# Kernel optimization log

Measured on AMD Instinct MI355X. Metric: run time of the kernel, lower is better.

The kernel has to match this reference:

```python
import jax, jax.numpy as jnp
import numpy as np

T, B, E = 2048, 2, 1024
H = 16
D = E // H


def setup_inputs() -> dict:
    key = jax.random.key(0)
    ks = jax.random.split(key, 7)
    s = 1.0 / np.sqrt(E)
    return {
        "query": jax.random.normal(ks[0], (T, B, E), jnp.float32),
        "key": jax.random.normal(ks[1], (T, B, E), jnp.float32),
        "value": jax.random.normal(ks[2], (T, B, E), jnp.float32),
        "in_proj_weight": jax.random.normal(ks[3], (3 * E, E), jnp.float32) * s,
        "in_proj_bias": jax.random.normal(ks[4], (3 * E,), jnp.float32) * 0.02,
        "out_proj_weight": jax.random.normal(ks[5], (E, E), jnp.float32) * s,
        "out_proj_bias": jax.random.normal(ks[6], (E,), jnp.float32) * 0.02,
    }


def reference(query, key, value, in_proj_weight, in_proj_bias, out_proj_weight, out_proj_bias):
    tgt_len, bsz, embed_dim = query.shape
    src_len = key.shape[0]
    head_dim = embed_dim // H
    # packed in-projection (F.linear: x @ W.T + b)
    w_q, w_k, w_v = jnp.split(in_proj_weight, 3, axis=0)
    b_q, b_k, b_v = jnp.split(in_proj_bias, 3, axis=0)
    q = query @ w_q.T + b_q   # [T, B, E]
    k = key @ w_k.T + b_k     # [S, B, E]
    v = value @ w_v.T + b_v   # [S, B, E]
    # [T,B,E] -> [B,H,T,D]
    q = q.reshape(tgt_len, bsz, H, head_dim).transpose(1, 2, 0, 3)
    k = k.reshape(src_len, bsz, H, head_dim).transpose(1, 2, 0, 3)
    v = v.reshape(src_len, bsz, H, head_dim).transpose(1, 2, 0, 3)
    scale = 1.0 / jnp.sqrt(jnp.asarray(head_dim, q.dtype))
    scores = jnp.einsum("bhtd,bhsd->bhts", q, k) * scale  # [B,H,T,S]
    attn_weights = jax.nn.softmax(scores, axis=-1)
    attn = jnp.einsum("bhts,bhsd->bhtd", attn_weights, v)  # [B,H,T,D]
    # [B,H,T,D] -> [T,B,E]
    attn = attn.transpose(2, 0, 1, 3).reshape(tgt_len, bsz, embed_dim)
    attn_output = attn @ out_proj_weight.T + out_proj_bias  # [T,B,E]
    # averaged attention weights over heads (average_attn_weights=True)
    avg_weights = jnp.sum(attn_weights, axis=1) / H  # [B,T,S]
    return attn_output, avg_weights
```

## Files before the change

kernel.cpp:

```cpp
#include <hip/hip_runtime.h>
#include <hip/hip_bf16.h>

typedef float  f32x2  __attribute__((ext_vector_type(2)));
typedef float  f32x4  __attribute__((ext_vector_type(4)));
typedef float  f32x16 __attribute__((ext_vector_type(16)));
typedef __bf16 bf16x8 __attribute__((ext_vector_type(8)));

#define MFMA16(A,B,C) __builtin_amdgcn_mfma_f32_16x16x32_bf16((A),(B),(C),0,0,0)
#define MFMA32(A,B,C) __builtin_amdgcn_mfma_f32_32x32x16_bf16((A),(B),(C),0,0,0)
#define EXP2(x) __builtin_amdgcn_exp2f(x)
#define LOG2(x) __builtin_amdgcn_logf(x)

static constexpr int Tn = 2048, Bn = 2, En = 1024, Hn = 16, Dn = 64;
static constexpr float kQScale = 0.125f * 1.4426950408889634f;

static __device__ __forceinline__ unsigned pack2(float a, float b) {
  union { __bf16 h[2]; unsigned u; } un;
  un.h[0] = (__bf16)a; un.h[1] = (__bf16)b;
  return un.u;
}

static __device__ __forceinline__ void gload_lds16(const void* g, void* l) {
  __builtin_amdgcn_global_load_lds(
      (const __attribute__((address_space(1))) void*)g,
      (__attribute__((address_space(3))) void*)l, 16, 0, 0);
}

__global__ __launch_bounds__(256)
void k_cvt(const float* __restrict__ q, const float* __restrict__ k,
           const float* __restrict__ v, const float* __restrict__ w3,
           const float* __restrict__ wo,
           __bf16* __restrict__ qb, __bf16* __restrict__ kb,
           __bf16* __restrict__ vb, __bf16* __restrict__ w3b,
           __bf16* __restrict__ wob)
{
  const size_t g = (size_t)blockIdx.x * 256 + threadIdx.x;
  const float* src;
  __bf16* dst;
  size_t off;
  if (g < 524288)        { src = q;  dst = qb;  off = g; }
  else if (g < 1048576)  { src = k;  dst = kb;  off = g - 524288; }
  else if (g < 1572864)  { src = v;  dst = vb;  off = g - 1048576; }
  else if (g < 1966080)  { src = w3; dst = w3b; off = g - 1572864; }
  else                   { src = wo; dst = wob; off = g - 1966080; }
  const float* p = src + off * 8;
  f32x4 a = *reinterpret_cast<const f32x4*>(p);
  f32x4 b = *reinterpret_cast<const f32x4*>(p + 4);
  bf16x8 o;
  #pragma unroll
  for (int e = 0; e < 4; ++e) { o[e] = (__bf16)a[e]; o[e + 4] = (__bf16)b[e]; }
  *reinterpret_cast<bf16x8*>(dst + off * 8) = o;
}

__global__ __launch_bounds__(256)
void k_qkv(const __bf16* __restrict__ Xq, const __bf16* __restrict__ Xk,
           const __bf16* __restrict__ Xv, const __bf16* __restrict__ W,
           const float* __restrict__ bias,
           __bf16* __restrict__ q_ws, __bf16* __restrict__ k_ws,
           __bf16* __restrict__ v_ws)
{
  __shared__ __align__(16) char a_lds[8192];
  __shared__ __align__(16) char b_lds[8192];
  const int tid = threadIdx.x;
  const int lane = tid & 63, w = tid >> 6;
  const int wr = w >> 1, wc = w & 1;
  const int ag = lane >> 4, lr = lane & 15;
  const int mBase = blockIdx.x * 128;
  const int oBase = blockIdx.y * 128;
  const int which = blockIdx.y >> 3;
  const __bf16* X  = (which == 0) ? Xq : ((which == 1) ? Xk : Xv);
  const __bf16* Wt = W + (size_t)oBase * En;
  __bf16* dst = (which == 0) ? q_ws : ((which == 1) ? k_ws : v_ws);
  const float oscale = (which == 0) ? kQScale : 1.0f;

  const int g0 = w >> 1, h0 = w & 1;
  const int gA = w;
  char* laA0 = a_lds + gA * 2048;
  char* laA1 = a_lds + gA * 2048 + 1024;
  char* lbA0 = b_lds + gA * 2048;
  char* lbA1 = b_lds + gA * 2048 + 1024;
  const __bf16* pa0 = X  + (size_t)(mBase + lane) * En + gA * 8;
  const __bf16* pa1 = X  + (size_t)(mBase + 64 + lane) * En + gA * 8;
  const __bf16* pb0 = Wt + (size_t)(lane) * En + gA * 8;
  const __bf16* pb1 = Wt + (size_t)(64 + lane) * En + gA * 8;
  (void)g0; (void)h0;

  f32x4 acc[4][4];
  #pragma unroll
  for (int i = 0; i < 4; ++i)
    #pragma unroll
    for (int j = 0; j < 4; ++j) { f32x4 z = {0.f, 0.f, 0.f, 0.f}; acc[i][j] = z; }

  for (int kk = 0; kk < En; kk += 32) {
    __syncthreads();
    gload_lds16(pa0 + kk, laA0);
    gload_lds16(pa1 + kk, laA1);
    gload_lds16(pb0 + kk, lbA0);
    gload_lds16(pb1 + kk, lbA1);
    __syncthreads();
    bf16x8 af[4], bfr[4];
    #pragma unroll
    for (int mb = 0; mb < 4; ++mb)
      af[mb] = *(const bf16x8*)(a_lds + ag * 2048 + (wr * 64 + mb * 16 + lr) * 16);
    #pragma unroll
    for (int nb = 0; nb < 4; ++nb)
      bfr[nb] = *(const bf16x8*)(b_lds + ag * 2048 + (wc * 64 + nb * 16 + lr) * 16);
    #pragma unroll
    for (int mb = 0; mb < 4; ++mb)
      #pragma unroll
      for (int nb = 0; nb < 4; ++nb)
        acc[mb][nb] = MFMA16(af[mb], bfr[nb], acc[mb][nb]);
  }

  #pragma unroll
  for (int nb = 0; nb < 4; ++nb) {
    int oG = oBase + wc * 64 + nb * 16 + lr;
    float bv = bias[oG];
    int oS = oG & (En - 1);
    int h = oS >> 6, d = oS & 63;
    #pragma unroll
    for (int mb = 0; mb < 4; ++mb)
      #pragma unroll
      for (int r = 0; r < 4; ++r) {
        int i = mBase + wr * 64 + mb * 16 + ag * 4 + r;
        int t = i >> 1, b2 = i & 1;
        dst[(((size_t)(b2 * Hn + h)) * Tn + t) * Dn + d] =
            (__bf16)((acc[mb][nb][r] + bv) * oscale);
      }
  }
}

__global__ __launch_bounds__(256)
void k_transpose_v(const __bf16* __restrict__ v_ws, __bf16* __restrict__ vt_ws)
{
  __shared__ __bf16 tile[64][72];
  const int bh = blockIdx.x >> 5;
  const int tt = blockIdx.x & 31;
  const int tid = threadIdx.x;
  const __bf16* src = v_ws + ((size_t)bh * Tn + tt * 64) * Dn;
  #pragma unroll
  for (int it = 0; it < 2; ++it) {
    int gi = tid + it * 256;
    int row = gi >> 3, gg = gi & 7;
    *reinterpret_cast<bf16x8*>(&tile[row][gg * 8]) =
        *reinterpret_cast<const bf16x8*>(src + row * Dn + gg * 8);
  }
  __syncthreads();
  __bf16* dst = vt_ws + (size_t)bh * Dn * Tn + tt * 64;
  #pragma unroll
  for (int it = 0; it < 2; ++it) {
    int gi = tid + it * 256;
    int drow = gi >> 3, tg = gi & 7;
    bf16x8 vv;
    #pragma unroll
    for (int e = 0; e < 8; ++e) vv[e] = tile[tg * 8 + e][drow];
    *reinterpret_cast<bf16x8*>(dst + (size_t)drow * Tn + tg * 8) = vv;
  }
}

__global__ __launch_bounds__(256, 2)
void k_flash(const __bf16* __restrict__ q_ws, const __bf16* __restrict__ k_ws,
             const __bf16* __restrict__ vt_ws, __bf16* __restrict__ ctx,
             float* __restrict__ stats)
{
  __shared__ __align__(16) char k_sm[8192];
  __shared__ __align__(16) char v_sm[8192];
  __shared__ __align__(16) float es_sm[4][32];

  const int tid = threadIdx.x;
  const int lane = tid & 63, w = tid >> 6;
  const int tl = lane & 31, hi = lane >> 5;
  const int bh = blockIdx.x >> 4;
  const int qt = blockIdx.x & 15;
  const int t0w = qt * 128 + w * 32;

  const __bf16* kbase  = k_ws + (size_t)bh * Tn * Dn;
  const __bf16* vtbase = vt_ws + (size_t)bh * Dn * Tn;

  bf16x8 qf[4];
  {
    const __bf16* qrow = q_ws + ((size_t)bh * Tn + t0w + tl) * Dn + hi * 8;
    #pragma unroll
    for (int c = 0; c < 4; ++c)
      qf[c] = *reinterpret_cast<const bf16x8*>(qrow + c * 16);
  }

  f32x16 accO0, accO1;
  #pragma unroll
  for (int i = 0; i < 16; ++i) { accO0[i] = 0.f; accO1[i] = 0.f; }
  float m_run = -INFINITY, l_run = 0.f;

  const int r0 = tid >> 3, s0 = tid & 7;
  const int ldso = ((s0 ^ (r0 & 7)) << 4);
  const int ko0 = r0 * 128 + ldso, ko1 = ko0 + 32 * 128;

  bf16x8 rk0 = *(const bf16x8*)(kbase + r0 * 64 + s0 * 8);
  bf16x8 rk1 = *(const bf16x8*)(kbase + (r0 + 32) * 64 + s0 * 8);
  bf16x8 rv0 = *(const bf16x8*)(vtbase + (size_t)r0 * Tn + s0 * 8);
  bf16x8 rv1 = *(const bf16x8*)(vtbase + (size_t)(r0 + 32) * Tn + s0 * 8);

  for (int st = 0; st < 32; ++st) {
    __syncthreads();
    *(bf16x8*)(k_sm + ko0) = rk0;
    *(bf16x8*)(k_sm + ko1) = rk1;
    *(bf16x8*)(v_sm + ko0) = rv0;
    *(bf16x8*)(v_sm + ko1) = rv1;
    __syncthreads();
    if (st + 1 < 32) {
      const __bf16* kn = kbase + (size_t)(st + 1) * 64 * Dn;
      const __bf16* vn = vtbase + (st + 1) * 64;
      rk0 = *(const bf16x8*)(kn + r0 * 64 + s0 * 8);
      rk1 = *(const bf16x8*)(kn + (r0 + 32) * 64 + s0 * 8);
      rv0 = *(const bf16x8*)(vn + (size_t)r0 * Tn + s0 * 8);
      rv1 = *(const bf16x8*)(vn + (size_t)(r0 + 32) * Tn + s0 * 8);
    }

    f32x16 sc0, sc1;
    #pragma unroll
    for (int i = 0; i < 16; ++i) { sc0[i] = 0.f; sc1[i] = 0.f; }
    const char* kr0 = k_sm + tl * 128;
    const char* kr1 = k_sm + (32 + tl) * 128;
    #pragma unroll
    for (int c = 0; c < 4; ++c) {
      const int off = (((2 * c + hi) ^ (tl & 7)) << 4);
      sc0 = MFMA32(*(const bf16x8*)(kr0 + off), qf[c], sc0);
      sc1 = MFMA32(*(const bf16x8*)(kr1 + off), qf[c], sc1);
    }

    float mx[8];
    #pragma unroll
    for (int i = 0; i < 8; ++i)
      mx[i] = fmaxf(fmaxf(sc0[i], sc0[i + 8]), fmaxf(sc1[i], sc1[i + 8]));
    float tm = fmaxf(fmaxf(fmaxf(mx[0], mx[1]), fmaxf(mx[2], mx[3])),
                     fmaxf(fmaxf(mx[4], mx[5]), fmaxf(mx[6], mx[7])));
    tm = fmaxf(tm, __shfl_xor(tm, 32, 64));
    const float mn = fmaxf(m_run, tm);
    const float es = EXP2(m_run - mn);
    m_run = mn;
    #pragma unroll
    for (int i = 0; i < 16; ++i) {
      sc0[i] = EXP2(sc0[i] - mn);
      sc1[i] = EXP2(sc1[i] - mn);
    }
    float p0s = 0.f, p1s = 0.f, p2s = 0.f, p3s = 0.f;
    #pragma unroll
    for (int i = 0; i < 16; i += 4) {
      p0s += sc0[i]     + sc1[i];
      p1s += sc0[i + 1] + sc1[i + 1];
      p2s += sc0[i + 2] + sc1[i + 2];
      p3s += sc0[i + 3] + sc1[i + 3];
    }
    float rs = (p0s + p1s) + (p2s + p3s);
    rs += __shfl_xor(rs, 32, 64);
    l_run = l_run * es + rs;

    es_sm[w][tl] = es;
    f32x4 esr[4];
    #pragma unroll
    for (int q = 0; q < 4; ++q)
      esr[q] = *(const f32x4*)&es_sm[w][8 * q + 4 * hi];
    #pragma unroll
    for (int q = 0; q < 4; ++q)
      #pragma unroll
      for (int rr = 0; rr < 4; ++rr) {
        accO0[q * 4 + rr] *= esr[q][rr];
        accO1[q * 4 + rr] *= esr[q][rr];
      }

    unsigned wA0[4], wB0[4], wA1[4], wB1[4];
    #pragma unroll
    for (int g = 0; g < 4; ++g) {
      wA0[g] = pack2(sc0[4 * g],     sc0[4 * g + 1]);
      wB0[g] = pack2(sc0[4 * g + 2], sc0[4 * g + 3]);
      wA1[g] = pack2(sc1[4 * g],     sc1[4 * g + 1]);
      wB1[g] = pack2(sc1[4 * g + 2], sc1[4 * g + 3]);
    }
    bf16x8 pa[2][2];
    #pragma unroll
    for (int sb = 0; sb < 2; ++sb) {
      const unsigned* WA = sb ? wA1 : wA0;
      const unsigned* WB = sb ? wB1 : wB0;
      #pragma unroll
      for (int c = 0; c < 2; ++c) {
        unsigned a0 = WA[2 * c], a1 = WA[2 * c + 1];
        unsigned b0 = WB[2 * c], b1 = WB[2 * c + 1];
        unsigned xa0 = __shfl_xor(a0, 32, 64);
        unsigned xa1 = __shfl_xor(a1, 32, 64);
        unsigned xb0 = __shfl_xor(b0, 32, 64);
        unsigned xb1 = __shfl_xor(b1, 32, 64);
        union { unsigned u[4]; bf16x8 v; } uu;
        uu.u[0] = hi ? xa1 : a0;
        uu.u[1] = hi ? xb1 : b0;
        uu.u[2] = hi ? a1 : xa0;
        uu.u[3] = hi ? b1 : xb0;
        pa[sb][c] = uu.v;
      }
    }

    const char* vr0 = v_sm + tl * 128;
    const char* vr1 = v_sm + (32 + tl) * 128;
    #pragma unroll
    for (int sb = 0; sb < 2; ++sb)
      #pragma unroll
      for (int c = 0; c < 2; ++c) {
        const int off = (((sb * 4 + c * 2 + hi) ^ (tl & 7)) << 4);
        accO0 = MFMA32(pa[sb][c], *(const bf16x8*)(vr0 + off), accO0);
        accO1 = MFMA32(pa[sb][c], *(const bf16x8*)(vr1 + off), accO1);
      }
  }

  const float linv = 1.0f / l_run;
  es_sm[w][tl] = linv;
  f32x4 lr[4];
  #pragma unroll
  for (int q = 0; q < 4; ++q)
    lr[q] = *(const f32x4*)&es_sm[w][8 * q + 4 * hi];
  const int b2 = bh >> 4, h = bh & 15;
  #pragma unroll
  for (int q = 0; q < 4; ++q)
    #pragma unroll
    for (int rr = 0; rr < 4; ++rr) {
      const int t = t0w + 8 * q + 4 * hi + rr;
      __bf16* cp = ctx + ((size_t)t * Bn + b2) * En + h * 64 + tl;
      cp[0]  = (__bf16)(accO0[q * 4 + rr] * lr[q][rr]);
      cp[32] = (__bf16)(accO1[q * 4 + rr] * lr[q][rr]);
    }
  if (hi == 0) {
    const int t = t0w + tl;
    f32x2 stv; stv[0] = m_run; stv[1] = l_run;
    *reinterpret_cast<f32x2*>(&stats[((size_t)bh * Tn + t) * 2]) = stv;
  }
}

__global__ __launch_bounds__(256)
void k_avgw(const __bf16* __restrict__ q_ws, const __bf16* __restrict__ k_ws,
            const float* __restrict__ stats, float* __restrict__ avg_out)
{
  __shared__ __align__(16) char q_sm[8192];
  __shared__ __align__(16) char k_sm[8192];
  __shared__ __align__(16) float adj_sm[16][64];

  const int tid = threadIdx.x;
  const int lane = tid & 63, w = tid >> 6;
  const int tl = lane & 31, hi = lane >> 5;
  const int b2 = blockIdx.x >> 10;
  const int tt = (blockIdx.x >> 5) & 31;
  const int ss = blockIdx.x & 31;
  const int thalf = (w >> 1) * 32, shalf = (w & 1) * 32;

  #pragma unroll
  for (int it = 0; it < 4; ++it) {
    int idx = tid + it * 256;
    int h = idx >> 6, trow = idx & 63;
    f32x2 sv = *(const f32x2*)&stats[(((size_t)(b2 * Hn + h)) * Tn + tt * 64 + trow) * 2];
    adj_sm[h][trow] = sv[0] + LOG2(16.0f * sv[1]);
  }

  const size_t hstride = (size_t)Tn * Dn;
  const __bf16* qb = q_ws + ((size_t)(b2 * Hn) * Tn + tt * 64) * Dn;
  const __bf16* kb = k_ws + ((size_t)(b2 * Hn) * Tn + ss * 64) * Dn;

  const int r0 = tid >> 3, s0 = tid & 7;
  const int ldso = ((s0 ^ (r0 & 7)) << 4);
  const int ko0 = r0 * 128 + ldso, ko1 = ko0 + 32 * 128;

  bf16x8 rq0 = *(const bf16x8*)(qb + r0 * 64 + s0 * 8);
  bf16x8 rq1 = *(const bf16x8*)(qb + (r0 + 32) * 64 + s0 * 8);
  bf16x8 rk0 = *(const bf16x8*)(kb + r0 * 64 + s0 * 8);
  bf16x8 rk1 = *(const bf16x8*)(kb + (r0 + 32) * 64 + s0 * 8);

  f32x16 avg;
  #pragma unroll
  for (int i = 0; i < 16; ++i) avg[i] = 0.f;

  const char* qr = q_sm + (thalf + tl) * 128;
  const char* kr = k_sm + (shalf + tl) * 128;

  for (int h = 0; h < Hn; ++h) {
    __syncthreads();
    *(bf16x8*)(q_sm + ko0) = rq0;
    *(bf16x8*)(q_sm + ko1) = rq1;
    *(bf16x8*)(k_sm + ko0) = rk0;
    *(bf16x8*)(k_sm + ko1) = rk1;
    __syncthreads();
    if (h + 1 < Hn) {
      const __bf16* qn = qb + (size_t)(h + 1) * hstride;
      const __bf16* kn = kb + (size_t)(h + 1) * hstride;
      rq0 = *(const bf16x8*)(qn + r0 * 64 + s0 * 8);
      rq1 = *(const bf16x8*)(qn + (r0 + 32) * 64 + s0 * 8);
      rk0 = *(const bf16x8*)(kn + r0 * 64 + s0 * 8);
      rk1 = *(const bf16x8*)(kn + (r0 + 32) * 64 + s0 * 8);
    }

    f32x16 sc;
    #pragma unroll
    for (int i = 0; i < 16; ++i) sc[i] = 0.f;
    #pragma unroll
    for (int c = 0; c < 4; ++c) {
      const int off = (((2 * c + hi) ^ (tl & 7)) << 4);
      sc = MFMA32(*(const bf16x8*)(qr + off), *(const bf16x8*)(kr + off), sc);
    }

    #pragma unroll
    for (int q = 0; q < 4; ++q) {
      f32x4 ad = *(const f32x4*)&adj_sm[h][thalf + 8 * q + 4 * hi];
      #pragma unroll
      for (int r = 0; r < 4; ++r)
        avg[q * 4 + r] += EXP2(sc[q * 4 + r] - ad[r]);
    }
  }

  #pragma unroll
  for (int q = 0; q < 4; ++q)
    #pragma unroll
    for (int r = 0; r < 4; ++r) {
      int t = tt * 64 + thalf + 8 * q + 4 * hi + r;
      int s = ss * 64 + shalf + tl;
      avg_out[((size_t)(b2 * Tn + t)) * Tn + s] = avg[q * 4 + r];
    }
}

__global__ __launch_bounds__(256)
void k_outproj(const __bf16* __restrict__ ctx, const __bf16* __restrict__ W,
               const float* __restrict__ bias, float* __restrict__ out)
{
  __shared__ __align__(16) char a_lds[8192];
  __shared__ __align__(16) char b_lds[8192];
  const int tid = threadIdx.x;
  const int lane = tid & 63, w = tid >> 6;
  const int wr = w >> 1, wc = w & 1;
  const int ag = lane >> 4, lr = lane & 15;
  const int mBase = blockIdx.x * 128;
  const int oBase = blockIdx.y * 128;
  const __bf16* Wt = W + (size_t)oBase * En;

  const int gA = w;
  char* laA0 = a_lds + gA * 2048;
  char* laA1 = a_lds + gA * 2048 + 1024;
  char* lbA0 = b_lds + gA * 2048;
  char* lbA1 = b_lds + gA * 2048 + 1024;
  const __bf16* pa0 = ctx + (size_t)(mBase + lane) * En + gA * 8;
  const __bf16* pa1 = ctx + (size_t)(mBase + 64 + lane) * En + gA * 8;
  const __bf16* pb0 = Wt + (size_t)(lane) * En + gA * 8;
  const __bf16* pb1 = Wt + (size_t)(64 + lane) * En + gA * 8;

  f32x4 acc[4][4];
  #pragma unroll
  for (int i = 0; i < 4; ++i)
    #pragma unroll
    for (int j = 0; j < 4; ++j) { f32x4 z = {0.f,0.f,0.f,0.f}; acc[i][j] = z; }

  for (int kk = 0; kk < En; kk += 32) {
    __syncthreads();
    gload_lds16(pa0 + kk, laA0);
    gload_lds16(pa1 + kk, laA1);
    gload_lds16(pb0 + kk, lbA0);
    gload_lds16(pb1 + kk, lbA1);
    __syncthreads();
    bf16x8 af[4], bfr[4];
    #pragma unroll
    for (int mb = 0; mb < 4; ++mb)
      af[mb] = *(const bf16x8*)(a_lds + ag * 2048 + (wr * 64 + mb * 16 + lr) * 16);
    #pragma unroll
    for (int nb = 0; nb < 4; ++nb)
      bfr[nb] = *(const bf16x8*)(b_lds + ag * 2048 + (wc * 64 + nb * 16 + lr) * 16);
    #pragma unroll
    for (int mb = 0; mb < 4; ++mb)
      #pragma unroll
      for (int nb = 0; nb < 4; ++nb)
        acc[mb][nb] = MFMA16(af[mb], bfr[nb], acc[mb][nb]);
  }

  #pragma unroll
  for (int nb = 0; nb < 4; ++nb) {
    int o = oBase + wc * 64 + nb * 16 + lr;
    float bv = bias[o];
    #pragma unroll
    for (int mb = 0; mb < 4; ++mb)
      #pragma unroll
      for (int r = 0; r < 4; ++r) {
        int i = mBase + wr * 64 + mb * 16 + ag * 4 + r;
        out[(size_t)i * En + o] = acc[mb][nb][r] + bv;
      }
  }
}

extern "C" void kernel_launch(void* const* d_in, const int* in_sizes, int n_in,
                              void* d_out, int out_size, void* d_ws, size_t ws_size,
                              hipStream_t stream)
{
  (void)in_sizes; (void)n_in; (void)out_size; (void)ws_size;
  const float* query = (const float*)d_in[0];
  const float* key   = (const float*)d_in[1];
  const float* value = (const float*)d_in[2];
  const float* in_w  = (const float*)d_in[3];
  const float* in_b  = (const float*)d_in[4];
  const float* out_w = (const float*)d_in[5];
  const float* out_b = (const float*)d_in[6];

  float* attn_out = (float*)d_out;
  float* avg_out  = (float*)d_out + (size_t)Tn * Bn * En;

  char* ws = (char*)d_ws;
  const size_t MB = 1u << 20;
  __bf16* q_ws  = (__bf16*)(ws);
  __bf16* k_ws  = (__bf16*)(ws + 8 * MB);
  __bf16* v_ws  = (__bf16*)(ws + 16 * MB);
  __bf16* vt_ws = (__bf16*)(ws + 24 * MB);
  __bf16* ctx   = (__bf16*)(ws + 32 * MB);
  float*  stats = (float*)(ws + 40 * MB);
  __bf16* xq_bf = vt_ws;
  __bf16* xk_bf = ctx;
  __bf16* xv_bf = (__bf16*)(ws + 40 * MB + 512 * 1024);
  __bf16* w3_bf = (__bf16*)(ws + 48 * MB + 512 * 1024);
  __bf16* wo_bf = (__bf16*)(ws + 54 * MB + 512 * 1024);

  k_cvt<<<8192, 256, 0, stream>>>(query, key, value, in_w, out_w,
                                  xq_bf, xk_bf, xv_bf, w3_bf, wo_bf);
  k_qkv<<<dim3(32, 24), 256, 0, stream>>>(xq_bf, xk_bf, xv_bf, w3_bf, in_b,
                                          q_ws, k_ws, v_ws);
  k_transpose_v<<<1024, 256, 0, stream>>>(v_ws, vt_ws);
  k_flash<<<512, 256, 0, stream>>>(q_ws, k_ws, vt_ws, ctx, stats);
  k_avgw<<<2048, 256, 0, stream>>>(q_ws, k_ws, stats, avg_out);
  k_outproj<<<dim3(32, 8), 256, 0, stream>>>(ctx, wo_bf, out_b, attn_out);
}
```

Baseline: 215.0 us.

## Double-buffer K/V LDS in flash kernel, lazy max rescale, shuffle-based scaling

```diff
diff --git a/kernel.cpp b/kernel.cpp
--- a/kernel.cpp
+++ b/kernel.cpp
@@ -73,7 +73,6 @@
   __bf16* dst = (which == 0) ? q_ws : ((which == 1) ? k_ws : v_ws);
   const float oscale = (which == 0) ? kQScale : 1.0f;
 
-  const int g0 = w >> 1, h0 = w & 1;
   const int gA = w;
   char* laA0 = a_lds + gA * 2048;
   char* laA1 = a_lds + gA * 2048 + 1024;
@@ -83,7 +82,6 @@
   const __bf16* pa1 = X  + (size_t)(mBase + 64 + lane) * En + gA * 8;
   const __bf16* pb0 = Wt + (size_t)(lane) * En + gA * 8;
   const __bf16* pb1 = Wt + (size_t)(64 + lane) * En + gA * 8;
-  (void)g0; (void)h0;
 
   f32x4 acc[4][4];
   #pragma unroll
@@ -163,9 +161,7 @@
              const __bf16* __restrict__ vt_ws, __bf16* __restrict__ ctx,
              float* __restrict__ stats)
 {
-  __shared__ __align__(16) char k_sm[8192];
-  __shared__ __align__(16) char v_sm[8192];
-  __shared__ __align__(16) float es_sm[4][32];
+  __shared__ __align__(16) char kv_sm[2 * 16384];
 
   const int tid = threadIdx.x;
   const int lane = tid & 63, w = tid >> 6;
@@ -192,20 +188,21 @@
 
   const int r0 = tid >> 3, s0 = tid & 7;
   const int ldso = ((s0 ^ (r0 & 7)) << 4);
-  const int ko0 = r0 * 128 + ldso, ko1 = ko0 + 32 * 128;
+  const int ko0 = r0 * 128 + ldso;
 
   bf16x8 rk0 = *(const bf16x8*)(kbase + r0 * 64 + s0 * 8);
   bf16x8 rk1 = *(const bf16x8*)(kbase + (r0 + 32) * 64 + s0 * 8);
   bf16x8 rv0 = *(const bf16x8*)(vtbase + (size_t)r0 * Tn + s0 * 8);
   bf16x8 rv1 = *(const bf16x8*)(vtbase + (size_t)(r0 + 32) * Tn + s0 * 8);
+  *(bf16x8*)(kv_sm + ko0) = rk0;
+  *(bf16x8*)(kv_sm + ko0 + 4096) = rk1;
+  *(bf16x8*)(kv_sm + 8192 + ko0) = rv0;
+  *(bf16x8*)(kv_sm + 8192 + ko0 + 4096) = rv1;
 
   for (int st = 0; st < 32; ++st) {
     __syncthreads();
-    *(bf16x8*)(k_sm + ko0) = rk0;
-    *(bf16x8*)(k_sm + ko1) = rk1;
-    *(bf16x8*)(v_sm + ko0) = rv0;
-    *(bf16x8*)(v_sm + ko1) = rv1;
-    __syncthreads();
+    const char* cur = kv_sm + (st & 1) * 16384;
+    char* nxt = kv_sm + ((st + 1) & 1) * 16384;
     if (st + 1 < 32) {
       const __bf16* kn = kbase + (size_t)(st + 1) * 64 * Dn;
       const __bf16* vn = vtbase + (st + 1) * 64;
@@ -218,14 +215,16 @@
     f32x16 sc0, sc1;
     #pragma unroll
     for (int i = 0; i < 16; ++i) { sc0[i] = 0.f; sc1[i] = 0.f; }
-    const char* kr0 = k_sm + tl * 128;
-    const char* kr1 = k_sm + (32 + tl) * 128;
+    const char* kr0 = cur + tl * 128;
+    const char* kr1 = cur + (32 + tl) * 128;
+    __builtin_amdgcn_s_setprio(1);
     #pragma unroll
     for (int c = 0; c < 4; ++c) {
       const int off = (((2 * c + hi) ^ (tl & 7)) << 4);
       sc0 = MFMA32(*(const bf16x8*)(kr0 + off), qf[c], sc0);
       sc1 = MFMA32(*(const bf16x8*)(kr1 + off), qf[c], sc1);
     }
+    __builtin_amdgcn_s_setprio(0);
 
     float mx[8];
     #pragma unroll
@@ -234,13 +233,24 @@
     float tm = fmaxf(fmaxf(fmaxf(mx[0], mx[1]), fmaxf(mx[2], mx[3])),
                      fmaxf(fmaxf(mx[4], mx[5]), fmaxf(mx[6], mx[7])));
     tm = fmaxf(tm, __shfl_xor(tm, 32, 64));
-    const float mn = fmaxf(m_run, tm);
-    const float es = EXP2(m_run - mn);
-    m_run = mn;
+    if (__any(tm > m_run + 8.0f)) {
+      const float mn = fmaxf(m_run, tm);
+      const float es = EXP2(m_run - mn);
+      m_run = mn;
+      l_run *= es;
+      #pragma unroll
+      for (int q = 0; q < 4; ++q)
+        #pragma unroll
+        for (int rr = 0; rr < 4; ++rr) {
+          const float e = __shfl(es, 8 * q + 4 * hi + rr, 32);
+          accO0[q * 4 + rr] *= e;
+          accO1[q * 4 + rr] *= e;
+        }
+    }
     #pragma unroll
     for (int i = 0; i < 16; ++i) {
-      sc0[i] = EXP2(sc0[i] - mn);
-      sc1[i] = EXP2(sc1[i] - mn);
+      sc0[i] = EXP2(sc0[i] - m_run);
+      sc1[i] = EXP2(sc1[i] - m_run);
     }
     float p0s = 0.f, p1s = 0.f, p2s = 0.f, p3s = 0.f;
     #pragma unroll
@@ -252,20 +262,7 @@
     }
     float rs = (p0s + p1s) + (p2s + p3s);
     rs += __shfl_xor(rs, 32, 64);
-    l_run = l_run * es + rs;
-
-    es_sm[w][tl] = es;
-    f32x4 esr[4];
-    #pragma unroll
-    for (int q = 0; q < 4; ++q)
-      esr[q] = *(const f32x4*)&es_sm[w][8 * q + 4 * hi];
-    #pragma unroll
-    for (int q = 0; q < 4; ++q)
-      #pragma unroll
-      for (int rr = 0; rr < 4; ++rr) {
-        accO0[q * 4 + rr] *= esr[q][rr];
-        accO1[q * 4 + rr] *= esr[q][rr];
-      }
+    l_run += rs;
 
     unsigned wA0[4], wB0[4], wA1[4], wB1[4];
     #pragma unroll
@@ -297,8 +294,9 @@
       }
     }
 
-    const char* vr0 = v_sm + tl * 128;
-    const char* vr1 = v_sm + (32 + tl) * 128;
+    const char* vr0 = cur + 8192 + tl * 128;
+    const char* vr1 = cur + 8192 + (32 + tl) * 128;
+    __builtin_amdgcn_s_setprio(1);
     #pragma unroll
     for (int sb = 0; sb < 2; ++sb)
       #pragma unroll
@@ -307,23 +305,27 @@
         accO0 = MFMA32(pa[sb][c], *(const bf16x8*)(vr0 + off), accO0);
         accO1 = MFMA32(pa[sb][c], *(const bf16x8*)(vr1 + off), accO1);
       }
+    __builtin_amdgcn_s_setprio(0);
+
+    if (st + 1 < 32) {
+      *(bf16x8*)(nxt + ko0) = rk0;
+      *(bf16x8*)(nxt + ko0 + 4096) = rk1;
+      *(bf16x8*)(nxt + 8192 + ko0) = rv0;
+      *(bf16x8*)(nxt + 8192 + ko0 + 4096) = rv1;
+    }
   }
 
   const float linv = 1.0f / l_run;
-  es_sm[w][tl] = linv;
-  f32x4 lr[4];
+  const int b2 = bh >> 4, h = bh & 15;
   #pragma unroll
   for (int q = 0; q < 4; ++q)
-    lr[q] = *(const f32x4*)&es_sm[w][8 * q + 4 * hi];
-  const int b2 = bh >> 4, h = bh & 15;
-  #pragma unroll
-  for (int q = 0; q < 4; ++q)
     #pragma unroll
     for (int rr = 0; rr < 4; ++rr) {
+      const float lv = __shfl(linv, 8 * q + 4 * hi + rr, 32);
       const int t = t0w + 8 * q + 4 * hi + rr;
       __bf16* cp = ctx + ((size_t)t * Bn + b2) * En + h * 64 + tl;
-      cp[0]  = (__bf16)(accO0[q * 4 + rr] * lr[q][rr]);
-      cp[32] = (__bf16)(accO1[q * 4 + rr] * lr[q][rr]);
+      cp[0]  = (__bf16)(accO0[q * 4 + rr] * lv);
+      cp[32] = (__bf16)(accO1[q * 4 + rr] * lv);
     }
   if (hi == 0) {
     const int t = t0w + tl;
```

After: 212.5 us. No clear change (-1.2%).
